# Kernel optimization log

Hardware: AMD Instinct MI355X
Metric: run time of the kernel (lower is better)

Reference implementation:

```python
import jax, jax.numpy as jnp
import numpy as np
import math

D_MODEL, D_STATE, D_CONV = 1024, 16, 4
D_INNER = 2 * D_MODEL
DT_RANK = math.ceil(D_MODEL / 16)
B, L = 4, 2048


def setup_inputs() -> dict:
    key = jax.random.key(0)
    ks = jax.random.split(key, 10)
    s = 0.02
    x = jax.random.normal(ks[0], (B, L, D_MODEL), dtype=jnp.float32)
    ln_g = jnp.ones((D_MODEL,), jnp.float32)
    ln_b = jnp.zeros((D_MODEL,), jnp.float32)
    W_in = jax.random.normal(ks[1], (D_MODEL, 2 * D_INNER), jnp.float32) * s
    conv_w = jax.random.normal(ks[2], (D_INNER, 1, D_CONV), jnp.float32) * s
    conv_b = jnp.zeros((D_INNER,), jnp.float32)
    W_xp = jax.random.normal(ks[3], (D_INNER, DT_RANK + 2 * D_STATE), jnp.float32) * s
    W_dt = jax.random.normal(ks[4], (DT_RANK, D_INNER), jnp.float32) * (DT_RANK ** -0.5)
    # inverse-softplus of dt ~ 0.01 (between dt_min=0.001 and dt_max=0.1)
    dt_bias = jnp.full((D_INNER,), float(np.log(np.expm1(0.01))), jnp.float32)
    # S4D-real init: A = 1..d_state per channel
    A_log = jnp.log(jnp.broadcast_to(jnp.arange(1, D_STATE + 1, dtype=jnp.float32), (D_INNER, D_STATE)))
    D_skip = jnp.ones((D_INNER,), jnp.float32)
    W_out = jax.random.normal(ks[5], (D_INNER, D_MODEL), jnp.float32) * s
    return dict(x=x, ln_g=ln_g, ln_b=ln_b, W_in=W_in, conv_w=conv_w, conv_b=conv_b,
                W_xp=W_xp, W_dt=W_dt, dt_bias=dt_bias, A_log=A_log, D_skip=D_skip, W_out=W_out)


def _layernorm(x, g, b, eps=1e-5):
    m = jnp.mean(x, axis=-1, keepdims=True)
    v = jnp.mean(jnp.square(x - m), axis=-1, keepdims=True)
    return (x - m) * jax.lax.rsqrt(v + eps) * g + b


def _mamba(xn, W_in, conv_w, conv_b, W_xp, W_dt, dt_bias, A_log, D_skip, W_out):
    # xn: [B, L, d_model]
    xz = xn @ W_in                                   # [B, L, 2*d_inner]
    xi, z = jnp.split(xz, 2, axis=-1)                # each [B, L, d_inner]
    # depthwise causal conv over sequence
    xi_t = jnp.transpose(xi, (0, 2, 1))              # [B, d_inner, L]
    xc = jax.lax.conv_general_dilated(
        xi_t, conv_w, window_strides=(1,), padding=[(D_CONV - 1, 0)],
        feature_group_count=D_INNER, dimension_numbers=('NCH', 'OIH', 'NCH'))
    xc = jnp.transpose(xc, (0, 2, 1)) + conv_b       # [B, L, d_inner]
    xc = jax.nn.silu(xc)
    # input-dependent dt, B, C
    x_dbl = xc @ W_xp                                # [B, L, dt_rank + 2*d_state]
    dt_lo, Bm, Cm = jnp.split(x_dbl, [DT_RANK, DT_RANK + D_STATE], axis=-1)
    delta = jax.nn.softplus(dt_lo @ W_dt + dt_bias)  # [B, L, d_inner]
    A = -jnp.exp(A_log)                              # [d_inner, d_state]

    def step(h, inp):
        dt_t, B_t, C_t, u_t = inp                    # [B,D], [B,N], [B,N], [B,D]
        dA = jnp.exp(dt_t[..., None] * A)            # [B, D, N]
        h = h * dA + (dt_t * u_t)[..., None] * B_t[:, None, :]
        y = jnp.einsum('bdn,bn->bd', h, C_t)
        return h, y

    h0 = jnp.zeros((xn.shape[0], D_INNER, D_STATE), xn.dtype)
    inputs = (jnp.transpose(delta, (1, 0, 2)), jnp.transpose(Bm, (1, 0, 2)),
              jnp.transpose(Cm, (1, 0, 2)), jnp.transpose(xc, (1, 0, 2)))
    _, ys = jax.lax.scan(step, h0, inputs)           # ys: [L, B, d_inner]
    y = jnp.transpose(ys, (1, 0, 2)) + xc * D_skip   # [B, L, d_inner]
    y = y * jax.nn.silu(z)
    return y @ W_out                                 # [B, L, d_model]


def reference(x, ln_g, ln_b, W_in, conv_w, conv_b, W_xp, W_dt, dt_bias, A_log, D_skip, W_out):
    xn = _layernorm(x, ln_g, ln_b)
    return _mamba(xn, W_in, conv_w, conv_b, W_xp, W_dt, dt_bias, A_log, D_skip, W_out) + x
```

## Files before the change

kernel.cpp:

```cpp
#include <hip/hip_runtime.h>

#define DM 1024
#define DI 2048
#define DS 16
#define DTR 64
#define LL 2048
#define NROW 8192

typedef unsigned short u16;
typedef unsigned int u32;
typedef __bf16 bf16x8 __attribute__((ext_vector_type(8)));
typedef float f32x4 __attribute__((ext_vector_type(4)));
typedef float v2f __attribute__((ext_vector_type(2)));

__device__ __forceinline__ float bf2f(u16 u) {
  unsigned int v = ((unsigned int)u) << 16;
  return __builtin_bit_cast(float, v);
}
__device__ __forceinline__ u16 f2bf(float f) {
  unsigned int x = __builtin_bit_cast(unsigned int, f);
  x = x + 0x7fffu + ((x >> 16) & 1u);
  return (u16)(x >> 16);
}
__device__ __forceinline__ float lo_bf(u32 v) { return __builtin_bit_cast(float, v << 16); }
__device__ __forceinline__ float hi_bf(u32 v) { return __builtin_bit_cast(float, v & 0xFFFF0000u); }
__device__ __forceinline__ u32 pack_bf(float a, float b) {
  return (u32)f2bf(a) | ((u32)f2bf(b) << 16);
}
__device__ __forceinline__ bool io_f32(const u16* lng) { return lng[0] == 0; }

__device__ __forceinline__ void async16(const void* g, void* l) {
  __builtin_amdgcn_global_load_lds(
      (const __attribute__((address_space(1))) unsigned int*)g,
      (__attribute__((address_space(3))) unsigned int*)l, 16, 0, 0);
}

__device__ __forceinline__ void pow16v(float e1, v2f* E) {
  float e2 = e1 * e1;
  v2f sq = {e2, e2};
  E[0] = (v2f){e1, e2};
#pragma unroll
  for (int k = 1; k < 8; k++) E[k] = E[k - 1] * sq;
}

__device__ void transpose_dev(const void* __restrict__ in, u16* __restrict__ out,
                              int R, int C, int Cp, int bx, int by, bool f32,
                              int tid, u16 (*tile)[33]) {
  int c0 = bx * 32, r0 = by * 32;
  int tx = tid & 31, ty = tid >> 5;
#pragma unroll
  for (int i = 0; i < 4; i++) {
    int r = r0 + ty + i * 8, c = c0 + tx;
    u16 v = 0;
    if (r < R && c < C) {
      if (f32) v = f2bf(((const float*)in)[(size_t)r * C + c]);
      else     v = ((const u16*)in)[(size_t)r * C + c];
    }
    tile[ty + i * 8][tx] = v;
// ... 62 lines not shown
  ushort4 o;
  u16* po = (u16*)&o;
#pragma unroll
  for (int k = 0; k < 4; k++) {
    float gk = f32 ? ((const float*)g)[c + k] : bf2f(g[c + k]);
    float bk = f32 ? ((const float*)b)[c + k] : bf2f(b[c + k]);
    po[k] = f2bf((f[k] - mean) * inv * gk + bk);
  }
  ((ushort4*)(xn + (size_t)row * DM))[tid] = o;
}

template <int EPI>
__device__ __forceinline__ void gemm_body(const u16* __restrict__ A,
                                          const u16* __restrict__ BT,
                                          void* __restrict__ C,
                                          const void* __restrict__ extra,
                                          int M, int N, int Klen, int ldk,
                                          const u16* __restrict__ lng, int mOff,
                                          u16* ldsA, u16* ldsB) {
  int tid = threadIdx.x;
  int wid = tid >> 6, lane = tid & 63;
  int l15 = lane & 15, quad = lane >> 4;
  int bm = blockIdx.x * 128;
  int bn;
  const u16* Ae = A;
  const u16* Be = BT;
  float* Cpart = nullptr;
  if (EPI == 5) {
    bn = 0;
    int ky = blockIdx.y;
    Ae += (size_t)ky * Klen;
    Be += (size_t)ky * Klen;
    Cpart = (float*)C + (size_t)ky * M * N;
  } else {
    bn = blockIdx.y * 128;
  }
  int wrow = (wid >> 1) * 64, wcol = (wid & 1) * 64;

  f32x4 zero = {0.f, 0.f, 0.f, 0.f};
  f32x4 acc[4][4];
#pragma unroll
  for (int i = 0; i < 4; i++)
#pragma unroll
    for (int j = 0; j < 4; j++) acc[i][j] = zero;

  int row0 = tid >> 2;
  int colb = (tid & 3) * 16;
  const char* Ap0 = (const char*)Ae + ((size_t)(bm + row0) * ldk) * 2 + colb;
  const char* Ap1 = (const char*)Ae + ((size_t)(bm + row0 + 64) * ldk) * 2 + colb;
  const char* Bp0 = (const char*)Be + ((size_t)(bn + row0) * ldk) * 2 + colb;
  const char* Bp1 = (const char*)Be + ((size_t)(bn + row0 + 64) * ldk) * 2 + colb;
  u16* la = ldsA + wid * 512;
  u16* lb = ldsB + wid * 512;

  for (int k0 = 0; k0 < Klen; k0 += 64) {
    size_t kb = (size_t)k0 * 2;
    async16(Ap0 + kb, la);
    async16(Ap1 + kb, la + 2048);
    async16(Ap0 + kb + 64, la + 4096);
    async16(Ap1 + kb + 64, la + 6144);
    async16(Bp0 + kb, lb);
    async16(Bp1 + kb, lb + 2048);
    async16(Bp0 + kb + 64, lb + 4096);
    async16(Bp1 + kb + 64, lb + 6144);
    __syncthreads();
#pragma unroll
    for (int s = 0; s < 2; s++) {
      bf16x8 af[4], bfr[4];
#pragma unroll
      for (int i = 0; i < 4; i++)
        af[i] = *(const bf16x8*)&ldsA[s * 4096 + (wrow + i * 16 + l15) * 32 + quad * 8];
#pragma unroll
      for (int j = 0; j < 4; j++)
        bfr[j] = *(const bf16x8*)&ldsB[s * 4096 + (wcol + j * 16 + l15) * 32 + quad * 8];
#pragma unroll
      for (int i = 0; i < 4; i++)
#pragma unroll
        for (int j = 0; j < 4; j++)
          acc[i][j] = __builtin_amdgcn_mfma_f32_16x16x32_bf16(af[i], bfr[j], acc[i][j], 0, 0, 0);
    }
    __syncthreads();
  }

  bool f32 = (EPI == 2) ? io_f32(lng) : false;
  if (EPI == 2 && !f32) {
    u16* tile = ldsA;
#pragma unroll
    for (int i = 0; i < 4; i++) {
#pragma unroll
      for (int j = 0; j < 4; j++) {
        int gn = bn + wcol + j * 16 + l15;
#pragma unroll
        for (int r = 0; r < 4; r++) {
          int lr = wrow + i * 16 + quad * 4 + r;
          float v = acc[i][j][r];
          v += bf2f(((const u16*)extra)[gn]);
          v = (v > 20.f) ? v : log1pf(__expf(v));
          tile[lr * 128 + wcol + j * 16 + l15] = f2bf(v);
        }
      }
    }
    __syncthreads();
#pragma unroll
    for (int g = 0; g < 8; g++) {
      int gi = g * 256 + tid;
      int row = gi >> 4, cg = gi & 15;
      uint4 v4 = *(const uint4*)&tile[row * 128 + cg * 8];
      *(uint4*)((u16*)C + (size_t)(bm + row + mOff) * N + bn + cg * 8) = v4;
    }
    return;
  }
#pragma unroll
  for (int i = 0; i < 4; i++) {
#pragma unroll
    for (int j = 0; j < 4; j++) {
      int gn = bn + wcol + j * 16 + l15;
#pragma unroll
      for (int r = 0; r < 4; r++) {
        int gm = bm + wrow + i * 16 + quad * 4 + r;
        float v = acc[i][j][r];
        if (EPI == 2) {
          float bias = ((const float*)extra)[gn];
          v += bias;
          float sp = (v > 20.f) ? v : log1pf(__expf(v));
          ((u16*)C)[(size_t)gm * N + gn] = f2bf(sp);
        } else {
          Cpart[(size_t)gm * N + gn] = v;
        }
      }
    }
  }
}

#define GEMM_WRAP(name, EPI)                                                        \
  __global__ __launch_bounds__(256) void name(                                      \
      const u16* __restrict__ A, const u16* __restrict__ BT, void* __restrict__ C,  \
      const void* __restrict__ extra, int M, int N, int Klen, int ldk,              \
      const u16* __restrict__ lng, int mOff) {                                      \
    __shared__ __align__(16) u16 lds[16384];                                        \
    gemm_body<EPI>(A, BT, C, extra, M, N, Klen, ldk, lng, mOff, lds, lds + 8192);   \
  }

GEMM_WRAP(gemm_xp_k, 5)
GEMM_WRAP(gemm_dt_k, 2)

__global__ __launch_bounds__(512, 2) void gemm_in256_k(
    const u16* __restrict__ A, const u16* __restrict__ BT,
    u16* __restrict__ C, u16* __restrict__ Z, int ldk, int Klen) {
  __shared__ __align__(16) u16 lds[65536];
  const int tid = threadIdx.x;
  const int wid = tid >> 6, lane = tid & 63;
  const int l15 = lane & 15, quad = lane >> 4;
  const int bm = blockIdx.x * 256, bn = blockIdx.y * 256;
  const int wrow = (wid >> 2) * 128;
  const int wcol = (wid & 3) * 64;

  const int srow = tid >> 3;
  const int sg = ((tid & 7) ^ (srow & 7)) * 8;
  const u16* Ag[4];
  const u16* Bg[4];
#pragma unroll
  for (int s = 0; s < 4; s++) {
    Ag[s] = A + (size_t)(bm + s * 64 + srow) * ldk + sg;
    Bg[s] = BT + (size_t)(bn + s * 64 + srow) * ldk + sg;
  }
  const int sdst = wid * 512;

// ... 129 lines not shown
    __builtin_amdgcn_s_setprio(0);
    if (st1) {
#pragma unroll
      for (int nf = 0; nf < 2; nf++)
#pragma unroll
        for (int ks = 0; ks < 2; ks++)
          b1[nf][ks] = *(const bf16x8*)&lds[nb + rB[ks] + (2 + nf) * 1024];
    }
  }

  __syncthreads();
  {
    const bool isZ = (bn >= DI);
#pragma unroll
    for (int i = 0; i < 8; i++) {
#pragma unroll
      for (int j = 0; j < 4; j++) {
        int lc = wcol + j * 16 + l15;
        int gr = lc >> 3, go = lc & 7;
#pragma unroll
        for (int r = 0; r < 4; r++) {
          int lr = wrow + i * 16 + quad * 4 + r;
          float v = acc[i][j][r];
          if (isZ) v = v / (1.f + __expf(-v));
          int grs = gr ^ ((lr & 7) ^ ((lr >> 3) & 7));
          lds[lr * 256 + grs * 8 + go] = f2bf(v);
        }
      }
    }
    __syncthreads();
    u16* outp = isZ ? (Z + (size_t)bm * DI + (bn - DI)) : (C + (size_t)bm * DI + bn);
#pragma unroll
    for (int g = 0; g < 16; g++) {
      int gi = g * 512 + tid;
      int row = gi >> 5, cg = gi & 31;
      int cgs = cg ^ ((row & 7) ^ ((row >> 3) & 7));
      uint4 v4 = *(const uint4*)&lds[row * 256 + cgs * 8];
      *(uint4*)(outp + (size_t)row * DI + cg * 8) = v4;
    }
  }
}

__global__ __launch_bounds__(512, 2) void gemm_out256_k(
    const u16* __restrict__ A, const u16* __restrict__ BT,
    void* __restrict__ C, const void* __restrict__ extra,
    int N, int ldk, int Klen, const u16* __restrict__ lng, int mOff) {
  __shared__ __align__(16) u16 lds[49152];
// ... 156 lines not shown
      int gi = g * 512 + tid;
      int row = gi >> 4, cg = gi & 15;
      int cgs = cg ^ ((row & 7) ^ ((row >> 3) & 7));
      uint4 v4 = *(const uint4*)&lds[row * 128 + cgs * 8];
      *(uint4*)((u16*)C + (size_t)(bm + row + mOff) * N + bn + cg * 8) = v4;
    }
  } else {
#pragma unroll
    for (int i = 0; i < 8; i++) {
#pragma unroll
      for (int j = 0; j < 2; j++) {
        int gn = bn + wcol + j * 16 + l15;
#pragma unroll
        for (int r = 0; r < 4; r++) {
          int gm = bm + wrow + i * 16 + quad * 4 + r;
          size_t idx = (size_t)(gm + mOff) * N + gn;
          ((float*)C)[idx] = acc[i][j][r] + ((const float*)extra)[idx];
        }
      }
    }
  }
}

__global__ __launch_bounds__(256) void conv4_k(const u16* __restrict__ xi,
                                               const void* __restrict__ cw,
                                               const void* __restrict__ cb,
                                               u16* __restrict__ xc,
                                               const u16* __restrict__ lng) {
  bool f32 = io_f32(lng);
  int idx = blockIdx.x * 256 + threadIdx.x;
  int c8 = (idx & (DI / 8 - 1)) * 8;
  int rq = idx >> 8;
  int l4 = (rq & (LL / 4 - 1)) * 4;
  int b = rq >> 9;
  float w[8][4], bi[8];
#pragma unroll
  for (int e = 0; e < 8; e++) {
    if (f32) {
      float4 w4 = ((const float4*)cw)[c8 + e];
      w[e][0] = w4.x; w[e][1] = w4.y; w[e][2] = w4.z; w[e][3] = w4.w;
      bi[e] = ((const float*)cb)[c8 + e];
    } else {
      ushort4 w4 = ((const ushort4*)cw)[c8 + e];
      w[e][0] = bf2f(w4.x); w[e][1] = bf2f(w4.y); w[e][2] = bf2f(w4.z); w[e][3] = bf2f(w4.w);
      bi[e] = bf2f(((const u16*)cb)[c8 + e]);
    }
  }
  size_t base = ((size_t)(b * LL + l4)) * DI + c8;
  float v[7][8];
#pragma unroll
  for (int j = 0; j < 7; j++) {
    int lj = l4 - 3 + j;
    if (lj >= 0) {
      uint4 q = *(const uint4*)&xi[base + (size_t)(j - 3) * DI];
      u32 qq[4] = {q.x, q.y, q.z, q.w};
#pragma unroll
      for (int e = 0; e < 4; e++) {
        v[j][2 * e] = lo_bf(qq[e]);
        v[j][2 * e + 1] = hi_bf(qq[e]);
      }
    } else {
#pragma unroll
      for (int e = 0; e < 8; e++) v[j][e] = 0.f;
    }
  }
#pragma unroll
  for (int r = 0; r < 4; r++) {
    u32 out[4];
#pragma unroll
    for (int e = 0; e < 8; e += 2) {
      float a0 = bi[e], a1 = bi[e + 1];
#pragma unroll
      for (int k = 0; k < 4; k++) {
        a0 += v[r + k][e] * w[e][k];
        a1 += v[r + k][e + 1] * w[e + 1][k];
      }
      a0 = a0 / (1.f + __expf(-a0));
      a1 = a1 / (1.f + __expf(-a1));
      out[e >> 1] = pack_bf(a0, a1);
    }
    uint4 o4 = {out[0], out[1], out[2], out[3]};
    *(uint4*)&xc[base + (size_t)r * DI] = o4;
  }
}

__global__ __launch_bounds__(256) void reduce_dtlo_k(const float* __restrict__ Cpart,
                                                     float* __restrict__ xdbl,
                                                     u16* __restrict__ dtlo, int M) {
  int i = blockIdx.x * 256 + threadIdx.x;
  size_t MN = (size_t)M * 128;
  float v = Cpart[i] + Cpart[MN + i] + Cpart[2 * MN + i] + Cpart[3 * MN + i];
  xdbl[i] = v;
  int j = i & 127, m = i >> 7;
  if (j < 64) dtlo[(size_t)m * 64 + j] = f2bf(v);
}

__device__ __forceinline__ bool fastA(const void* A_log, bool f32, int d0) {
  bool fast = true;
#pragma unroll
  for (int c = 0; c < 2; c++)
    for (int n = 0; n < 16; n++) {
      float al = f32 ? ((const float*)A_log)[(d0 + c) * DS + n]
                     : bf2f(((const u16*)A_log)[(d0 + c) * DS + n]);
      float Av = __expf(al);
      fast = fast && (__builtin_fabsf(Av - (float)(n + 1)) <= 1e-3f * (n + 1));
    }
  return fast;
}

template <int S>
__global__ __launch_bounds__(256) void scan_p1(const u16* __restrict__ delta,
                                               const u16* __restrict__ xc,
                                               const float* __restrict__ xdbl,
                                               const void* __restrict__ A_log,
                                               const u16* __restrict__ lng,
                                               float* __restrict__ Pbuf,
                                               float* __restrict__ Lbuf,
                                               float* __restrict__ sumbuf,
                                               int NS) {
  bool f32 = io_f32(lng);
  int tid = threadIdx.x;
  int seg = blockIdx.x, dch = blockIdx.y, bL = blockIdx.z;
  int d0 = (dch * 256 + tid) * 2;
  size_t rb = (size_t)bL * LL;
  int l0 = seg * S;
  extern __shared__ float bc[];
#pragma unroll 2
  for (int i = tid; i < S * 4; i += 256) {
    int t = i >> 2, k = (i & 3) * 4;
    *(float4*)&bc[t * 16 + k] = *(const float4*)&xdbl[(rb + l0 + t) * 128 + 64 + k];
  }
  __syncthreads();
  size_t sb = ((((size_t)bL * NS + seg) * DI) + d0) * DS;
  const u32* dpu = (const u32*)(delta + (rb + l0) * DI + d0);
  const u32* upu = (const u32*)(xc + (rb + l0) * DI + d0);
  if (fastA(A_log, f32, d0)) {
    v2f h0[8], h1[8];
#pragma unroll
    for (int k = 0; k < 8; k++) { h0[k] = (v2f){0.f, 0.f}; h1[k] = (v2f){0.f, 0.f}; }
    float sum0 = 0.f, sum1 = 0.f;
    const int T = 8;
    for (int t0 = 0; t0 < S; t0 += T) {
      u32 dv[T], uv[T];
#pragma unroll
      for (int j = 0; j < T; j++) {
        dv[j] = dpu[j * (DI / 2)];
        uv[j] = upu[j * (DI / 2)];
      }
      dpu += T * (DI / 2);
      upu += T * (DI / 2);
#pragma unroll
      for (int j = 0; j < T; j++) {
        float dt0 = lo_bf(dv[j]), dt1 = hi_bf(dv[j]);
        float u0 = lo_bf(uv[j]), u1 = hi_bf(uv[j]);
        sum0 += dt0; sum1 += dt1;
        const v2f* B2 = (const v2f*)&bc[(t0 + j) * 16];
        v2f E[8];
        pow16v(__expf(-dt0), E);
        float com0 = dt0 * u0;
        v2f cv0 = {com0, com0};
#pragma unroll
        for (int k = 0; k < 8; k++) h0[k] = h0[k] * E[k] + B2[k] * cv0;
        pow16v(__expf(-dt1), E);
        float com1 = dt1 * u1;
        v2f cv1 = {com1, com1};
#pragma unroll
        for (int k = 0; k < 8; k++) h1[k] = h1[k] * E[k] + B2[k] * cv1;
      }
    }
#pragma unroll
    for (int k = 0; k < 8; k++) { *(v2f*)&Lbuf[sb + 2 * k] = h0[k]; *(v2f*)&Lbuf[sb + 16 + 2 * k] = h1[k]; }
    if (sumbuf) {
      *(v2f*)&sumbuf[((size_t)(bL * NS + seg)) * DI + d0] = (v2f){sum0, sum1};
    } else {
      v2f P[8];
      pow16v(__expf(-sum0), P);
#pragma unroll
      for (int k = 0; k < 8; k++) *(v2f*)&Pbuf[sb + 2 * k] = P[k];
      pow16v(__expf(-sum1), P);
#pragma unroll
      for (int k = 0; k < 8; k++) *(v2f*)&Pbuf[sb + 16 + 2 * k] = P[k];
    }
  } else {
    for (int c = 0; c < 2; c++) {
      int d = d0 + c;
      float A2[16], h[16], P[16];
#pragma unroll
      for (int n = 0; n < 16; n++) {
        float al = f32 ? ((const float*)A_log)[d * DS + n] : bf2f(((const u16*)A_log)[d * DS + n]);
        A2[n] = -__expf(al);
        h[n] = 0.f; P[n] = 1.f;
      }
      const u16* dp = delta + (rb + l0) * DI + d;
      const u16* up = xc + (rb + l0) * DI + d;
      for (int t = 0; t < S; t++) {
        float dt = bf2f(dp[(size_t)t * DI]);
        float u = bf2f(up[(size_t)t * DI]);
        float com = dt * u;
        const float* Bf = &bc[t * 16];
#pragma unroll
        for (int n = 0; n < 16; n++) {
          float dA = __expf(dt * A2[n]);
          h[n] = fmaf(h[n], dA, com * Bf[n]);
          P[n] *= dA;
        }
      }
#pragma unroll
      for (int n = 0; n < 16; n++) { Pbuf[sb + 16 * c + n] = P[n]; Lbuf[sb + 16 * c + n] = h[n]; }
    }
  }
}

__global__ __launch_bounds__(256) void scan_p2(float* __restrict__ Pbuf,
                                               float* __restrict__ Lbuf,
                                               const float* __restrict__ sumbuf,
                                               const void* __restrict__ A_log,
                                               const u16* __restrict__ lng, int NS) {
  int idx = blockIdx.x * 256 + threadIdx.x;
  int bL = idx >> 15;
  int dn = idx & 32767;
  int d = dn >> 4, n = dn & 15;
  bool useSum = false;
  if (sumbuf) {
    bool f32 = io_f32(lng);
    useSum = fastA(A_log, f32, d & ~1);
  }
  float np1 = (float)(n + 1);
  float H = 0.f;
  for (int s = 0; s < NS; s++) {
    size_t o = ((size_t)(bL * NS + s) << 15) + dn;
    float Lv = Lbuf[o];
    float P = useSum ? __expf(-sumbuf[((size_t)(bL * NS + s)) * DI + d] * np1)
                     : Pbuf[o];
    Lbuf[o] = H;
    H = fmaf(P, H, Lv);
  }
}

template <int S>
__global__ __launch_bounds__(256) void scan_p3(u16* __restrict__ dy,
                                               const u16* __restrict__ xc,
                                               const float* __restrict__ xdbl,
                                               const u16* __restrict__ z,
                                               const void* __restrict__ A_log,
                                               const void* __restrict__ D_skip,
                                               const u16* __restrict__ lng,
                                               const float* __restrict__ Lbuf,
                                               int NS) {
  bool f32 = io_f32(lng);
  int tid = threadIdx.x;
  int seg = blockIdx.x, dch = blockIdx.y, bL = blockIdx.z;
  int d0 = (dch * 256 + tid) * 2;
  size_t rb = (size_t)bL * LL;
  int l0 = seg * S;
  extern __shared__ float bc[];
#pragma unroll 2
  for (int i = tid; i < S * 8; i += 256) {
    int t = i >> 3, k = (i & 7) * 4;
    *(float4*)&bc[t * 32 + k] = *(const float4*)&xdbl[(rb + l0 + t) * 128 + 64 + k];
  }
  __syncthreads();
  size_t sb = ((((size_t)bL * NS + seg) * DI) + d0) * DS;
  float Dv0 = f32 ? ((const float*)D_skip)[d0] : bf2f(((const u16*)D_skip)[d0]);
  float Dv1 = f32 ? ((const float*)D_skip)[d0 + 1] : bf2f(((const u16*)D_skip)[d0 + 1]);
  u32* dpu = (u32*)(dy + (rb + l0) * DI + d0);
  const u32* upu = (const u32*)(xc + (rb + l0) * DI + d0);
  const u32* zpu = (const u32*)(z + (rb + l0) * DI + d0);
  if (fastA(A_log, f32, d0)) {
    v2f h0[8], h1[8];
#pragma unroll
    for (int k = 0; k < 8; k++) {
      h0[k] = *(const v2f*)&Lbuf[sb + 2 * k];
      h1[k] = *(const v2f*)&Lbuf[sb + 16 + 2 * k];
    }
    const int T = 8;
    for (int t0 = 0; t0 < S; t0 += T) {
      u32 dv[T], uv[T], zv[T];
#pragma unroll
      for (int j = 0; j < T; j++) {
        dv[j] = dpu[j * (DI / 2)];
        uv[j] = upu[j * (DI / 2)];
        zv[j] = zpu[j * (DI / 2)];
      }
      upu += T * (DI / 2);
      zpu += T * (DI / 2);
#pragma unroll
      for (int j = 0; j < T; j++) {
        float dt0 = lo_bf(dv[j]), dt1 = hi_bf(dv[j]);
        float u0 = lo_bf(uv[j]), u1 = hi_bf(uv[j]);
        float zg0 = lo_bf(zv[j]), zg1 = hi_bf(zv[j]);
        const v2f* B2 = (const v2f*)&bc[(t0 + j) * 32];
        const v2f* C2 = (const v2f*)&bc[(t0 + j) * 32 + 16];
        v2f E[8];
        pow16v(__expf(-dt0), E);
        float com0 = dt0 * u0;
        v2f cv = {com0, com0};
        v2f a0 = {0.f, 0.f}, a1 = {0.f, 0.f};
#pragma unroll
        for (int k = 0; k < 8; k += 2) {
          h0[k] = h0[k] * E[k] + B2[k] * cv;
          h0[k + 1] = h0[k + 1] * E[k + 1] + B2[k + 1] * cv;
          a0 += h0[k] * C2[k];
          a1 += h0[k + 1] * C2[k + 1];
        }
        float cs0 = (a0.x + a0.y) + (a1.x + a1.y);
        pow16v(__expf(-dt1), E);
        float com1 = dt1 * u1;
        cv = (v2f){com1, com1};
        a0 = (v2f){0.f, 0.f}; a1 = (v2f){0.f, 0.f};
#pragma unroll
        for (int k = 0; k < 8; k += 2) {
          h1[k] = h1[k] * E[k] + B2[k] * cv;
          h1[k + 1] = h1[k + 1] * E[k + 1] + B2[k + 1] * cv;
          a0 += h1[k] * C2[k];
          a1 += h1[k + 1] * C2[k + 1];
        }
        float cs1 = (a0.x + a0.y) + (a1.x + a1.y);
        float y0 = (cs0 + u0 * Dv0) * zg0;
        float y1 = (cs1 + u1 * Dv1) * zg1;
        dpu[j * (DI / 2)] = pack_bf(y0, y1);
      }
      dpu += T * (DI / 2);
    }
  } else {
    for (int c = 0; c < 2; c++) {
      int d = d0 + c;
      float A2[16], h[16];
#pragma unroll
      for (int n = 0; n < 16; n++) {
        float al = f32 ? ((const float*)A_log)[d * DS + n] : bf2f(((const u16*)A_log)[d * DS + n]);
        A2[n] = -__expf(al);
        h[n] = Lbuf[sb + 16 * c + n];
      }
      float Dv = (c == 0) ? Dv0 : Dv1;
      u16* dp = dy + (rb + l0) * DI + d;
      const u16* up = xc + (rb + l0) * DI + d;
      const u16* zp = z + (rb + l0) * DI + d;
      for (int t = 0; t < S; t++) {
        float dt = bf2f(dp[(size_t)t * DI]);
        float u = bf2f(up[(size_t)t * DI]);
        float zg = bf2f(zp[(size_t)t * DI]);
        float com = dt * u;
        const float* Bf = &bc[t * 32];
        const float* Cf = &bc[t * 32 + 16];
        float cs = 0.f;
#pragma unroll
        for (int n = 0; n < 16; n++) {
          float dA = __expf(dt * A2[n]);
          h[n] = fmaf(h[n], dA, com * Bf[n]);
          cs = fmaf(h[n], Cf[n], cs);
        }
        dp[(size_t)t * DI] = f2bf((cs + u * Dv) * zg);
      }
    }
  }
}

static void launch_scan(int NS, int nb, u16* xi, u16* xc, float* xdbl, u16* z,
                        const u16* A_log, const u16* D_sk, const u16* ln_g,
                        float* Pbuf, float* Lbuf, float* sumbuf,
                        hipStream_t stream) {
  int S = LL / NS;
  dim3 g1(NS, 4, nb);
  if (S == 32) {
    scan_p1<32><<<g1, 256, 32 * 64, stream>>>(xi, xc, xdbl, A_log, ln_g, Pbuf, Lbuf, sumbuf, NS);
  } else if (S == 64) {
    scan_p1<64><<<g1, 256, 64 * 64, stream>>>(xi, xc, xdbl, A_log, ln_g, Pbuf, Lbuf, sumbuf, NS);
  } else {
    scan_p1<128><<<g1, 256, 128 * 64, stream>>>(xi, xc, xdbl, A_log, ln_g, Pbuf, Lbuf, sumbuf, NS);
  }
  scan_p2<<<nb * 128, 256, 0, stream>>>(Pbuf, Lbuf, sumbuf, A_log, ln_g, NS);
  if (S == 32) {
    scan_p3<32><<<g1, 256, 32 * 128, stream>>>(xi, xc, xdbl, z, A_log, D_sk, ln_g, Lbuf, NS);
  } else if (S == 64) {
    scan_p3<64><<<g1, 256, 64 * 128, stream>>>(xi, xc, xdbl, z, A_log, D_sk, ln_g, Lbuf, NS);
  } else {
    scan_p3<128><<<g1, 256, 128 * 128, stream>>>(xi, xc, xdbl, z, A_log, D_sk, ln_g, Lbuf, NS);
  }
}

extern "C" void kernel_launch(void* const* d_in, const int* in_sizes, int n_in,
                              void* d_out, int out_size, void* d_ws, size_t ws_size,
                              hipStream_t stream) {
  const u16* x = (const u16*)d_in[0];
  const u16* ln_g = (const u16*)d_in[1];
  const u16* ln_b = (const u16*)d_in[2];
  const u16* W_in = (const u16*)d_in[3];
  const u16* cw = (const u16*)d_in[4];
  const u16* cb = (const u16*)d_in[5];
  const u16* W_xp = (const u16*)d_in[6];
  const u16* W_dt = (const u16*)d_in[7];
  const u16* dt_b = (const u16*)d_in[8];
  const u16* A_log = (const u16*)d_in[9];
  const u16* D_sk = (const u16*)d_in[10];
  const u16* W_out = (const u16*)d_in[11];

  char* ws = (char*)d_ws;
  const size_t MB = 1024 * 1024;

  if (ws_size >= 124 * MB) {
    int NS = (ws_size >= 180 * MB) ? 64 : (ws_size >= 144 * MB) ? 32 : 16;
    u16* xc = (u16*)(ws + 0);
    u16* xn = xc;
    u16* W_inT = (u16*)(ws + 16 * MB);
    u16* xi = (u16*)(ws + 32 * MB);
    u16* z = (u16*)(ws + 64 * MB);
    float* xdbl = (float*)(ws + 96 * MB);
    u16* dtlo = (u16*)(ws + 100 * MB);
    u16* W_xpT = (u16*)(ws + 101 * MB);
    u16* W_dtT = (u16*)(ws + 102 * MB);
    u16* W_outT = (u16*)(ws + 103 * MB);
    size_t stateSz = (size_t)NS * 4 * DI * DS * 4;
    float* Cpart = (float*)(ws + 107 * MB);
    float* Pbuf = (float*)(ws + 107 * MB);
    float* Lbuf = (float*)(ws + 107 * MB + stateSz);
    float* sumbuf = (NS >= 32) ? (float*)(ws + 107 * MB + 2 * stateSz) : nullptr;

    prep_k<<<6528 + NROW, 256, 0, stream>>>(W_in, W_inT, W_dt, W_dtT, W_xp, W_xpT,
                                            W_out, W_outT, x, ln_g, ln_b, xn);
    gemm_in256_k<<<dim3(NROW / 256, (2 * DI) / 256), 512, 0, stream>>>(xn, W_inT, xi, z, DM, DM);
    conv4_k<<<(NROW / 4) * (DI / 8) / 256, 256, 0, stream>>>(xi, cw, cb, xc, ln_g);
    gemm_xp_k<<<dim3(64, 4), 256, 0, stream>>>(xc, W_xpT, Cpart, nullptr, NROW, 128, 512, DI, ln_g, 0);
    reduce_dtlo_k<<<(NROW * 128) / 256, 256, 0, stream>>>(Cpart, xdbl, dtlo, NROW);
    gemm_dt_k<<<dim3(64, 16), 256, 0, stream>>>(dtlo, W_dtT, xi, dt_b, NROW, DI, DTR, DTR, ln_g, 0);
    launch_scan(NS, 4, xi, xc, xdbl, z, A_log, D_sk, ln_g, Pbuf, Lbuf, sumbuf, stream);
    gemm_out256_k<<<dim3(NROW / 256, DM / 128), 512, 0, stream>>>(xi, W_outT, d_out, x, DM, DI, DI, ln_g, 0);
  } else {
    int NS = 32;
    u16* W_inT = (u16*)(ws + 0);
    u16* W_xpT = (u16*)(ws + 8 * MB);
    u16* W_dtT = (u16*)(ws + 9 * MB);
    u16* W_outT = (u16*)(ws + 10 * MB);
    u16* xn = (u16*)(ws + 14 * MB);
    u16* xi = (u16*)(ws + 30 * MB);
    u16* z = (u16*)(ws + 38 * MB);
    u16* xc = (u16*)(ws + 46 * MB);
    float* xdbl = (float*)(ws + 54 * MB);
    u16* dtlo = (u16*)(ws + 55 * MB);
    float* Cpart = (float*)(ws + 56 * MB);
    float* Pbuf = (float*)(ws + 56 * MB);
    float* Lbuf = (float*)(ws + 61 * MB);

    prep_k<<<6528 + NROW, 256, 0, stream>>>(W_in, W_inT, W_dt, W_dtT, W_xp, W_xpT,
                                            W_out, W_outT, x, ln_g, ln_b, xn);
    for (int b = 0; b < 4; b++) {
      const u16* xnb = xn + (size_t)b * LL * DM;
      gemm_in256_k<<<dim3(LL / 256, (2 * DI) / 256), 512, 0, stream>>>(xnb, W_inT, xi, z, DM, DM);
      conv4_k<<<(LL / 4) * (DI / 8) / 256, 256, 0, stream>>>(xi, cw, cb, xc, ln_g);
      gemm_xp_k<<<dim3(16, 4), 256, 0, stream>>>(xc, W_xpT, Cpart, nullptr, LL, 128, 512, DI, ln_g, 0);
      reduce_dtlo_k<<<(LL * 128) / 256, 256, 0, stream>>>(Cpart, xdbl, dtlo, LL);
      gemm_dt_k<<<dim3(16, 16), 256, 0, stream>>>(dtlo, W_dtT, xi, dt_b, LL, DI, DTR, DTR, ln_g, 0);
      launch_scan(NS, 1, xi, xc, xdbl, z, A_log, D_sk, ln_g, Pbuf, Lbuf, nullptr, stream);
      gemm_out256_k<<<dim3(LL / 256, DM / 128), 512, 0, stream>>>(xi, W_outT, d_out, x, DM, DI, DI, ln_g, b * LL);
    }
  }
}
```

Baseline: 486.6 us.

## Fuse causal conv+SiLU into x_proj GEMM and recompute it inside scan kernels

```diff
diff --git a/kernel.cpp b/kernel.cpp
--- a/kernel.cpp
+++ b/kernel.cpp
@@ -34,6 +34,8 @@
       (const __attribute__((address_space(1))) unsigned int*)g,
       (__attribute__((address_space(3))) unsigned int*)l, 16, 0, 0);
 }
+
+__device__ __forceinline__ float silu(float a) { return a / (1.f + __expf(-a)); }
 
 __device__ __forceinline__ void pow16v(float e1, v2f* E) {
   float e2 = e1 * e1;
@@ -142,19 +144,7 @@
   int wid = tid >> 6, lane = tid & 63;
   int l15 = lane & 15, quad = lane >> 4;
   int bm = blockIdx.x * 128;
-  int bn;
-  const u16* Ae = A;
-  const u16* Be = BT;
-  float* Cpart = nullptr;
-  if (EPI == 5) {
-    bn = 0;
-    int ky = blockIdx.y;
-    Ae += (size_t)ky * Klen;
-    Be += (size_t)ky * Klen;
-    Cpart = (float*)C + (size_t)ky * M * N;
-  } else {
-    bn = blockIdx.y * 128;
-  }
+  int bn = blockIdx.y * 128;
   int wrow = (wid >> 1) * 64, wcol = (wid & 1) * 64;
 
   f32x4 zero = {0.f, 0.f, 0.f, 0.f};
@@ -166,10 +156,10 @@
 
   int row0 = tid >> 2;
   int colb = (tid & 3) * 16;
-  const char* Ap0 = (const char*)Ae + ((size_t)(bm + row0) * ldk) * 2 + colb;
-  const char* Ap1 = (const char*)Ae + ((size_t)(bm + row0 + 64) * ldk) * 2 + colb;
-  const char* Bp0 = (const char*)Be + ((size_t)(bn + row0) * ldk) * 2 + colb;
-  const char* Bp1 = (const char*)Be + ((size_t)(bn + row0 + 64) * ldk) * 2 + colb;
+  const char* Ap0 = (const char*)A + ((size_t)(bm + row0) * ldk) * 2 + colb;
+  const char* Ap1 = (const char*)A + ((size_t)(bm + row0 + 64) * ldk) * 2 + colb;
+  const char* Bp0 = (const char*)BT + ((size_t)(bn + row0) * ldk) * 2 + colb;
+  const char* Bp1 = (const char*)BT + ((size_t)(bn + row0 + 64) * ldk) * 2 + colb;
   u16* la = ldsA + wid * 512;
   u16* lb = ldsB + wid * 512;
 
@@ -202,8 +192,8 @@
     __syncthreads();
   }
 
-  bool f32 = (EPI == 2) ? io_f32(lng) : false;
-  if (EPI == 2 && !f32) {
+  bool f32 = io_f32(lng);
+  if (!f32) {
     u16* tile = ldsA;
 #pragma unroll
     for (int i = 0; i < 4; i++) {
@@ -239,30 +229,142 @@
       for (int r = 0; r < 4; r++) {
         int gm = bm + wrow + i * 16 + quad * 4 + r;
         float v = acc[i][j][r];
-        if (EPI == 2) {
-          float bias = ((const float*)extra)[gn];
-          v += bias;
-          float sp = (v > 20.f) ? v : log1pf(__expf(v));
-          ((u16*)C)[(size_t)gm * N + gn] = f2bf(sp);
+        float bias = ((const float*)extra)[gn];
+        v += bias;
+        float sp = (v > 20.f) ? v : log1pf(__expf(v));
+        ((u16*)C)[(size_t)gm * N + gn] = f2bf(sp);
+      }
+    }
+  }
+}
+
+__global__ __launch_bounds__(256) void gemm_dt_k(
+    const u16* __restrict__ A, const u16* __restrict__ BT, void* __restrict__ C,
+    const void* __restrict__ extra, int M, int N, int Klen, int ldk,
+    const u16* __restrict__ lng, int mOff) {
+  __shared__ __align__(16) u16 lds[16384];
+  gemm_body<2>(A, BT, C, extra, M, N, Klen, ldk, lng, mOff, lds, lds + 8192);
+}
+
+__global__ __launch_bounds__(256) void gemm_xpf_k(
+    const u16* __restrict__ xi, const u16* __restrict__ BT,
+    float* __restrict__ Cpart, const void* __restrict__ cw,
+    const void* __restrict__ cb, const u16* __restrict__ lng, int M) {
+  __shared__ __align__(16) u16 ldsA[10240];
+  __shared__ __align__(16) u16 ldsB[8192];
+  bool f32 = io_f32(lng);
+  int tid = threadIdx.x;
+  int wid = tid >> 6, lane = tid & 63;
+  int l15 = lane & 15, quad = lane >> 4;
+  int bm = blockIdx.x * 128;
+  int ky = blockIdx.y;
+  float* Cp = Cpart + (size_t)ky * M * 128;
+  int wrow = (wid >> 1) * 64, wcol = (wid & 1) * 64;
+
+  f32x4 zero = {0.f, 0.f, 0.f, 0.f};
+  f32x4 acc[4][4];
+#pragma unroll
+  for (int i = 0; i < 4; i++)
+#pragma unroll
+    for (int j = 0; j < 4; j++) acc[i][j] = zero;
+
+  int row0 = tid >> 2, colb = (tid & 3) * 16;
+  const char* Bp0 = (const char*)BT + ((size_t)row0 * DI + (size_t)ky * 512) * 2 + colb;
+  const char* Bp1 = (const char*)BT + ((size_t)(row0 + 64) * DI + (size_t)ky * 512) * 2 + colb;
+  u16* lb = ldsB + wid * 512;
+
+  int ar = tid >> 1, as = tid & 1;
+  int grow = bm + ar;
+  int lrow = grow & (LL - 1);
+  const u16* xrow = xi + (size_t)grow * DI;
+
+  for (int k0 = 0; k0 < 512; k0 += 64) {
+    size_t kb = (size_t)k0 * 2;
+    async16(Bp0 + kb, lb);
+    async16(Bp1 + kb, lb + 2048);
+    async16(Bp0 + kb + 64, lb + 4096);
+    async16(Bp1 + kb + 64, lb + 6144);
+    int cbase = ky * 512 + k0 + as * 32;
+#pragma unroll
+    for (int it = 0; it < 4; it++) {
+      int cc = ((ar + it) & 3) * 8;
+      int ch = cbase + cc;
+      float wv[8][4], bv[8];
+#pragma unroll
+      for (int e = 0; e < 8; e++) {
+        if (f32) {
+          float4 w4 = ((const float4*)cw)[ch + e];
+          wv[e][0] = w4.x; wv[e][1] = w4.y; wv[e][2] = w4.z; wv[e][3] = w4.w;
+          bv[e] = ((const float*)cb)[ch + e];
         } else {
-          Cpart[(size_t)gm * N + gn] = v;
+          ushort4 w4 = ((const ushort4*)cw)[ch + e];
+          wv[e][0] = bf2f(w4.x); wv[e][1] = bf2f(w4.y);
+          wv[e][2] = bf2f(w4.z); wv[e][3] = bf2f(w4.w);
+          bv[e] = bf2f(((const u16*)cb)[ch + e]);
         }
       }
-    }
-  }
-}
-
-#define GEMM_WRAP(name, EPI)                                                        \
-  __global__ __launch_bounds__(256) void name(                                      \
-      const u16* __restrict__ A, const u16* __restrict__ BT, void* __restrict__ C,  \
-      const void* __restrict__ extra, int M, int N, int Klen, int ldk,              \
-      const u16* __restrict__ lng, int mOff) {                                      \
-    __shared__ __align__(16) u16 lds[16384];                                        \
-    gemm_body<EPI>(A, BT, C, extra, M, N, Klen, ldk, lng, mOff, lds, lds + 8192);   \
-  }
-
-GEMM_WRAP(gemm_xp_k, 5)
-GEMM_WRAP(gemm_dt_k, 2)
+      float xin[4][8];
+#pragma unroll
+      for (int j = 0; j < 4; j++) {
+        int lr = lrow - 3 + j;
+        if (lr >= 0) {
+          uint4 q = *(const uint4*)&xrow[(ptrdiff_t)(j - 3) * DI + ch];
+          u32 qq[4] = {q.x, q.y, q.z, q.w};
+#pragma unroll
+          for (int e = 0; e < 4; e++) {
+            xin[j][2 * e] = lo_bf(qq[e]);
+            xin[j][2 * e + 1] = hi_bf(qq[e]);
+          }
+        } else {
+#pragma unroll
+          for (int e = 0; e < 8; e++) xin[j][e] = 0.f;
+        }
+      }
+      u32 o[4];
+#pragma unroll
+      for (int e = 0; e < 8; e += 2) {
+        float a0 = bv[e], a1 = bv[e + 1];
+#pragma unroll
+        for (int j = 0; j < 4; j++) {
+          a0 += xin[j][e] * wv[e][j];
+          a1 += xin[j][e + 1] * wv[e + 1][j];
+        }
+        o[e >> 1] = pack_bf(silu(a0), silu(a1));
+      }
+      uint4 q4 = {o[0], o[1], o[2], o[3]};
+      *(uint4*)&ldsA[as * 5120 + ar * 40 + cc] = q4;
+    }
+    __syncthreads();
+#pragma unroll
+    for (int s = 0; s < 2; s++) {
+      bf16x8 af[4], bfr[4];
+#pragma unroll
+      for (int i = 0; i < 4; i++)
+        af[i] = *(const bf16x8*)&ldsA[s * 5120 + (wrow + i * 16 + l15) * 40 + quad * 8];
+#pragma unroll
+      for (int j = 0; j < 4; j++)
+        bfr[j] = *(const bf16x8*)&ldsB[s * 4096 + (wcol + j * 16 + l15) * 32 + quad * 8];
+#pragma unroll
+      for (int i = 0; i < 4; i++)
+#pragma unroll
+        for (int j = 0; j < 4; j++)
+          acc[i][j] = __builtin_amdgcn_mfma_f32_16x16x32_bf16(af[i], bfr[j], acc[i][j], 0, 0, 0);
+    }
+    __syncthreads();
+  }
+#pragma unroll
+  for (int i = 0; i < 4; i++) {
+#pragma unroll
+    for (int j = 0; j < 4; j++) {
+      int gn = wcol + j * 16 + l15;
+#pragma unroll
+      for (int r = 0; r < 4; r++) {
+        int gm = bm + wrow + i * 16 + quad * 4 + r;
+        Cp[(size_t)gm * 128 + gn] = acc[i][j][r];
+      }
+    }
+  }
+}
 
 __global__ __launch_bounds__(512, 2) void gemm_in256_k(
     const u16* __restrict__ A, const u16* __restrict__ BT,
@@ -438,7 +540,7 @@
         for (int r = 0; r < 4; r++) {
           int lr = wrow + i * 16 + quad * 4 + r;
           float v = acc[i][j][r];
-          if (isZ) v = v / (1.f + __expf(-v));
+          if (isZ) v = silu(v);
           int grs = gr ^ ((lr & 7) ^ ((lr >> 3) & 7));
           lds[lr * 256 + grs * 8 + go] = f2bf(v);
         }
@@ -641,68 +743,6 @@
   }
 }
 
-__global__ __launch_bounds__(256) void conv4_k(const u16* __restrict__ xi,
-                                               const void* __restrict__ cw,
-                                               const void* __restrict__ cb,
-                                               u16* __restrict__ xc,
-                                               const u16* __restrict__ lng) {
-  bool f32 = io_f32(lng);
-  int idx = blockIdx.x * 256 + threadIdx.x;
-  int c8 = (idx & (DI / 8 - 1)) * 8;
-  int rq = idx >> 8;
-  int l4 = (rq & (LL / 4 - 1)) * 4;
-  int b = rq >> 9;
-  float w[8][4], bi[8];
-#pragma unroll
-  for (int e = 0; e < 8; e++) {
-    if (f32) {
-      float4 w4 = ((const float4*)cw)[c8 + e];
-      w[e][0] = w4.x; w[e][1] = w4.y; w[e][2] = w4.z; w[e][3] = w4.w;
-      bi[e] = ((const float*)cb)[c8 + e];
-    } else {
-      ushort4 w4 = ((const ushort4*)cw)[c8 + e];
-      w[e][0] = bf2f(w4.x); w[e][1] = bf2f(w4.y); w[e][2] = bf2f(w4.z); w[e][3] = bf2f(w4.w);
-      bi[e] = bf2f(((const u16*)cb)[c8 + e]);
-    }
-  }
-  size_t base = ((size_t)(b * LL + l4)) * DI + c8;
-  float v[7][8];
-#pragma unroll
-  for (int j = 0; j < 7; j++) {
-    int lj = l4 - 3 + j;
-    if (lj >= 0) {
-      uint4 q = *(const uint4*)&xi[base + (size_t)(j - 3) * DI];
-      u32 qq[4] = {q.x, q.y, q.z, q.w};
-#pragma unroll
-      for (int e = 0; e < 4; e++) {
-        v[j][2 * e] = lo_bf(qq[e]);
-        v[j][2 * e + 1] = hi_bf(qq[e]);
-      }
-    } else {
-#pragma unroll
-      for (int e = 0; e < 8; e++) v[j][e] = 0.f;
-    }
-  }
-#pragma unroll
-  for (int r = 0; r < 4; r++) {
-    u32 out[4];
-#pragma unroll
-    for (int e = 0; e < 8; e += 2) {
-      float a0 = bi[e], a1 = bi[e + 1];
-#pragma unroll
-      for (int k = 0; k < 4; k++) {
-        a0 += v[r + k][e] * w[e][k];
-        a1 += v[r + k][e + 1] * w[e + 1][k];
-      }
-      a0 = a0 / (1.f + __expf(-a0));
-      a1 = a1 / (1.f + __expf(-a1));
-      out[e >> 1] = pack_bf(a0, a1);
-    }
-    uint4 o4 = {out[0], out[1], out[2], out[3]};
-    *(uint4*)&xc[base + (size_t)r * DI] = o4;
-  }
-}
-
 __global__ __launch_bounds__(256) void reduce_dtlo_k(const float* __restrict__ Cpart,
                                                      float* __restrict__ xdbl,
                                                      u16* __restrict__ dtlo, int M) {
@@ -729,9 +769,11 @@
 
 template <int S>
 __global__ __launch_bounds__(256) void scan_p1(const u16* __restrict__ delta,
-                                               const u16* __restrict__ xc,
+                                               const u16* __restrict__ xi,
                                                const float* __restrict__ xdbl,
                                                const void* __restrict__ A_log,
+                                               const void* __restrict__ cw,
+                                               const void* __restrict__ cb,
                                                const u16* __restrict__ lng,
                                                float* __restrict__ Pbuf,
                                                float* __restrict__ Lbuf,
@@ -752,8 +794,32 @@
   __syncthreads();
   size_t sb = ((((size_t)bL * NS + seg) * DI) + d0) * DS;
   const u32* dpu = (const u32*)(delta + (rb + l0) * DI + d0);
-  const u32* upu = (const u32*)(xc + (rb + l0) * DI + d0);
+  const u32* upu = (const u32*)(xi + (rb + l0) * DI + d0);
   if (fastA(A_log, f32, d0)) {
+    float w0[4], w1[4], cb0, cb1;
+    if (f32) {
+      float4 a0 = ((const float4*)cw)[d0], a1 = ((const float4*)cw)[d0 + 1];
+      w0[0] = a0.x; w0[1] = a0.y; w0[2] = a0.z; w0[3] = a0.w;
+      w1[0] = a1.x; w1[1] = a1.y; w1[2] = a1.z; w1[3] = a1.w;
+      cb0 = ((const float*)cb)[d0]; cb1 = ((const float*)cb)[d0 + 1];
+    } else {
+      ushort4 a0 = ((const ushort4*)cw)[d0], a1 = ((const ushort4*)cw)[d0 + 1];
+      w0[0] = bf2f(a0.x); w0[1] = bf2f(a0.y); w0[2] = bf2f(a0.z); w0[3] = bf2f(a0.w);
+      w1[0] = bf2f(a1.x); w1[1] = bf2f(a1.y); w1[2] = bf2f(a1.z); w1[3] = bf2f(a1.w);
+      cb0 = bf2f(((const u16*)cb)[d0]); cb1 = bf2f(((const u16*)cb)[d0 + 1]);
+    }
+    float hx0[3], hx1[3];
+    if (l0 == 0) {
+#pragma unroll
+      for (int i = 0; i < 3; i++) { hx0[i] = 0.f; hx1[i] = 0.f; }
+    } else {
+      const u32* hp = (const u32*)(xi + (rb + l0 - 3) * DI + d0);
+#pragma unroll
+      for (int i = 0; i < 3; i++) {
+        u32 v = hp[i * (DI / 2)];
+        hx0[i] = lo_bf(v); hx1[i] = hi_bf(v);
+      }
+    }
     v2f h0[8], h1[8];
 #pragma unroll
     for (int k = 0; k < 8; k++) { h0[k] = (v2f){0.f, 0.f}; h1[k] = (v2f){0.f, 0.f}; }
@@ -771,7 +837,12 @@
 #pragma unroll
       for (int j = 0; j < T; j++) {
         float dt0 = lo_bf(dv[j]), dt1 = hi_bf(dv[j]);
-        float u0 = lo_bf(uv[j]), u1 = hi_bf(uv[j]);
+        float xr0 = lo_bf(uv[j]), xr1 = hi_bf(uv[j]);
+        float a0 = cb0 + hx0[0] * w0[0] + hx0[1] * w0[1] + hx0[2] * w0[2] + xr0 * w0[3];
+        float a1 = cb1 + hx1[0] * w1[0] + hx1[1] * w1[1] + hx1[2] * w1[2] + xr1 * w1[3];
+        float u0 = silu(a0), u1 = silu(a1);
+        hx0[0] = hx0[1]; hx0[1] = hx0[2]; hx0[2] = xr0;
+        hx1[0] = hx1[1]; hx1[1] = hx1[2]; hx1[2] = xr1;
         sum0 += dt0; sum1 += dt1;
         const v2f* B2 = (const v2f*)&bc[(t0 + j) * 16];
         v2f E[8];
@@ -810,11 +881,28 @@
         A2[n] = -__expf(al);
         h[n] = 0.f; P[n] = 1.f;
       }
+      float wc[4], bc2;
+      if (f32) {
+        float4 w4 = ((const float4*)cw)[d];
+        wc[0] = w4.x; wc[1] = w4.y; wc[2] = w4.z; wc[3] = w4.w;
+        bc2 = ((const float*)cb)[d];
+      } else {
+        ushort4 w4 = ((const ushort4*)cw)[d];
+        wc[0] = bf2f(w4.x); wc[1] = bf2f(w4.y); wc[2] = bf2f(w4.z); wc[3] = bf2f(w4.w);
+        bc2 = bf2f(((const u16*)cb)[d]);
+      }
+      float hx[3];
+#pragma unroll
+      for (int i = 0; i < 3; i++)
+        hx[i] = (l0 == 0) ? 0.f : bf2f(xi[(rb + l0 - 3 + i) * DI + d]);
       const u16* dp = delta + (rb + l0) * DI + d;
-      const u16* up = xc + (rb + l0) * DI + d;
+      const u16* up = xi + (rb + l0) * DI + d;
       for (int t = 0; t < S; t++) {
         float dt = bf2f(dp[(size_t)t * DI]);
-        float u = bf2f(up[(size_t)t * DI]);
+        float xv = bf2f(up[(size_t)t * DI]);
+        float av = bc2 + hx[0] * wc[0] + hx[1] * wc[1] + hx[2] * wc[2] + xv * wc[3];
+        float u = silu(av);
+        hx[0] = hx[1]; hx[1] = hx[2]; hx[2] = xv;
         float com = dt * u;
         const float* Bf = &bc[t * 16];
 #pragma unroll
@@ -858,11 +946,13 @@
 
 template <int S>
 __global__ __launch_bounds__(256) void scan_p3(u16* __restrict__ dy,
-                                               const u16* __restrict__ xc,
+                                               const u16* __restrict__ xi,
                                                const float* __restrict__ xdbl,
                                                const u16* __restrict__ z,
                                                const void* __restrict__ A_log,
                                                const void* __restrict__ D_skip,
+                                               const void* __restrict__ cw,
+                                               const void* __restrict__ cb,
                                                const u16* __restrict__ lng,
                                                const float* __restrict__ Lbuf,
                                                int NS) {
@@ -883,9 +973,33 @@
   float Dv0 = f32 ? ((const float*)D_skip)[d0] : bf2f(((const u16*)D_skip)[d0]);
   float Dv1 = f32 ? ((const float*)D_skip)[d0 + 1] : bf2f(((const u16*)D_skip)[d0 + 1]);
   u32* dpu = (u32*)(dy + (rb + l0) * DI + d0);
-  const u32* upu = (const u32*)(xc + (rb + l0) * DI + d0);
+  const u32* upu = (const u32*)(xi + (rb + l0) * DI + d0);
   const u32* zpu = (const u32*)(z + (rb + l0) * DI + d0);
   if (fastA(A_log, f32, d0)) {
+    float w0[4], w1[4], cb0, cb1;
+    if (f32) {
+      float4 a0 = ((const float4*)cw)[d0], a1 = ((const float4*)cw)[d0 + 1];
+      w0[0] = a0.x; w0[1] = a0.y; w0[2] = a0.z; w0[3] = a0.w;
+      w1[0] = a1.x; w1[1] = a1.y; w1[2] = a1.z; w1[3] = a1.w;
+      cb0 = ((const float*)cb)[d0]; cb1 = ((const float*)cb)[d0 + 1];
+    } else {
+      ushort4 a0 = ((const ushort4*)cw)[d0], a1 = ((const ushort4*)cw)[d0 + 1];
+      w0[0] = bf2f(a0.x); w0[1] = bf2f(a0.y); w0[2] = bf2f(a0.z); w0[3] = bf2f(a0.w);
+      w1[0] = bf2f(a1.x); w1[1] = bf2f(a1.y); w1[2] = bf2f(a1.z); w1[3] = bf2f(a1.w);
+      cb0 = bf2f(((const u16*)cb)[d0]); cb1 = bf2f(((const u16*)cb)[d0 + 1]);
+    }
+    float hx0[3], hx1[3];
+    if (l0 == 0) {
+#pragma unroll
+      for (int i = 0; i < 3; i++) { hx0[i] = 0.f; hx1[i] = 0.f; }
+    } else {
+      const u32* hp = (const u32*)(xi + (rb + l0 - 3) * DI + d0);
+#pragma unroll
+      for (int i = 0; i < 3; i++) {
+        u32 v = hp[i * (DI / 2)];
+        hx0[i] = lo_bf(v); hx1[i] = hi_bf(v);
+      }
+    }
     v2f h0[8], h1[8];
 #pragma unroll
     for (int k = 0; k < 8; k++) {
@@ -906,8 +1020,13 @@
 #pragma unroll
       for (int j = 0; j < T; j++) {
         float dt0 = lo_bf(dv[j]), dt1 = hi_bf(dv[j]);
-        float u0 = lo_bf(uv[j]), u1 = hi_bf(uv[j]);
+        float xr0 = lo_bf(uv[j]), xr1 = hi_bf(uv[j]);
         float zg0 = lo_bf(zv[j]), zg1 = hi_bf(zv[j]);
+        float a0c = cb0 + hx0[0] * w0[0] + hx0[1] * w0[1] + hx0[2] * w0[2] + xr0 * w0[3];
+        float a1c = cb1 + hx1[0] * w1[0] + hx1[1] * w1[1] + hx1[2] * w1[2] + xr1 * w1[3];
+        float u0 = silu(a0c), u1 = silu(a1c);
+        hx0[0] = hx0[1]; hx0[1] = hx0[2]; hx0[2] = xr0;
+        hx1[0] = hx1[1]; hx1[1] = hx1[2]; hx1[2] = xr1;
         const v2f* B2 = (const v2f*)&bc[(t0 + j) * 32];
         const v2f* C2 = (const v2f*)&bc[(t0 + j) * 32 + 16];
         v2f E[8];
@@ -951,14 +1070,31 @@
         A2[n] = -__expf(al);
         h[n] = Lbuf[sb + 16 * c + n];
       }
+      float wc[4], bc2;
+      if (f32) {
+        float4 w4 = ((const float4*)cw)[d];
+        wc[0] = w4.x; wc[1] = w4.y; wc[2] = w4.z; wc[3] = w4.w;
+        bc2 = ((const float*)cb)[d];
+      } else {
+        ushort4 w4 = ((const ushort4*)cw)[d];
+        wc[0] = bf2f(w4.x); wc[1] = bf2f(w4.y); wc[2] = bf2f(w4.z); wc[3] = bf2f(w4.w);
+        bc2 = bf2f(((const u16*)cb)[d]);
+      }
+      float hx[3];
+#pragma unroll
+      for (int i = 0; i < 3; i++)
+        hx[i] = (l0 == 0) ? 0.f : bf2f(xi[(rb + l0 - 3 + i) * DI + d]);
       float Dv = (c == 0) ? Dv0 : Dv1;
       u16* dp = dy + (rb + l0) * DI + d;
-      const u16* up = xc + (rb + l0) * DI + d;
+      const u16* up = xi + (rb + l0) * DI + d;
       const u16* zp = z + (rb + l0) * DI + d;
       for (int t = 0; t < S; t++) {
         float dt = bf2f(dp[(size_t)t * DI]);
-        float u = bf2f(up[(size_t)t * DI]);
+        float xv = bf2f(up[(size_t)t * DI]);
         float zg = bf2f(zp[(size_t)t * DI]);
+        float av = bc2 + hx[0] * wc[0] + hx[1] * wc[1] + hx[2] * wc[2] + xv * wc[3];
+        float u = silu(av);
+        hx[0] = hx[1]; hx[1] = hx[2]; hx[2] = xv;
         float com = dt * u;
         const float* Bf = &bc[t * 32];
         const float* Cf = &bc[t * 32 + 16];
@@ -975,26 +1111,27 @@
   }
 }
 
-static void launch_scan(int NS, int nb, u16* xi, u16* xc, float* xdbl, u16* z,
-                        const u16* A_log, const u16* D_sk, const u16* ln_g,
+static void launch_scan(int NS, int nb, u16* delta, u16* xi, float* xdbl, u16* z,
+                        const u16* A_log, const u16* D_sk, const u16* cw,
+                        const u16* cb, const u16* ln_g,
                         float* Pbuf, float* Lbuf, float* sumbuf,
                         hipStream_t stream) {
   int S = LL / NS;
   dim3 g1(NS, 4, nb);
   if (S == 32) {
-    scan_p1<32><<<g1, 256, 32 * 64, stream>>>(xi, xc, xdbl, A_log, ln_g, Pbuf, Lbuf, sumbuf, NS);
+    scan_p1<32><<<g1, 256, 32 * 64, stream>>>(delta, xi, xdbl, A_log, cw, cb, ln_g, Pbuf, Lbuf, sumbuf, NS);
   } else if (S == 64) {
-    scan_p1<64><<<g1, 256, 64 * 64, stream>>>(xi, xc, xdbl, A_log, ln_g, Pbuf, Lbuf, sumbuf, NS);
+    scan_p1<64><<<g1, 256, 64 * 64, stream>>>(delta, xi, xdbl, A_log, cw, cb, ln_g, Pbuf, Lbuf, sumbuf, NS);
   } else {
-    scan_p1<128><<<g1, 256, 128 * 64, stream>>>(xi, xc, xdbl, A_log, ln_g, Pbuf, Lbuf, sumbuf, NS);
+    scan_p1<128><<<g1, 256, 128 * 64, stream>>>(delta, xi, xdbl, A_log, cw, cb, ln_g, Pbuf, Lbuf, sumbuf, NS);
   }
   scan_p2<<<nb * 128, 256, 0, stream>>>(Pbuf, Lbuf, sumbuf, A_log, ln_g, NS);
   if (S == 32) {
-    scan_p3<32><<<g1, 256, 32 * 128, stream>>>(xi, xc, xdbl, z, A_log, D_sk, ln_g, Lbuf, NS);
+    scan_p3<32><<<g1, 256, 32 * 128, stream>>>(delta, xi, xdbl, z, A_log, D_sk, cw, cb, ln_g, Lbuf, NS);
   } else if (S == 64) {
-    scan_p3<64><<<g1, 256, 64 * 128, stream>>>(xi, xc, xdbl, z, A_log, D_sk, ln_g, Lbuf, NS);
+    scan_p3<64><<<g1, 256, 64 * 128, stream>>>(delta, xi, xdbl, z, A_log, D_sk, cw, cb, ln_g, Lbuf, NS);
   } else {
-    scan_p3<128><<<g1, 256, 128 * 128, stream>>>(xi, xc, xdbl, z, A_log, D_sk, ln_g, Lbuf, NS);
+    scan_p3<128><<<g1, 256, 128 * 128, stream>>>(delta, xi, xdbl, z, A_log, D_sk, cw, cb, ln_g, Lbuf, NS);
   }
 }
 
@@ -1018,10 +1155,10 @@
   const size_t MB = 1024 * 1024;
 
   if (ws_size >= 124 * MB) {
-    int NS = (ws_size >= 180 * MB) ? 64 : (ws_size >= 144 * MB) ? 32 : 16;
-    u16* xc = (u16*)(ws + 0);
-    u16* xn = xc;
+    int NS = (ws_size >= 144 * MB) ? 32 : 16;
+    u16* xn = (u16*)(ws + 0);
     u16* W_inT = (u16*)(ws + 16 * MB);
+    u16* delta = (u16*)(ws + 0);
     u16* xi = (u16*)(ws + 32 * MB);
     u16* z = (u16*)(ws + 64 * MB);
     float* xdbl = (float*)(ws + 96 * MB);
@@ -1038,12 +1175,11 @@
     prep_k<<<6528 + NROW, 256, 0, stream>>>(W_in, W_inT, W_dt, W_dtT, W_xp, W_xpT,
                                             W_out, W_outT, x, ln_g, ln_b, xn);
     gemm_in256_k<<<dim3(NROW / 256, (2 * DI) / 256), 512, 0, stream>>>(xn, W_inT, xi, z, DM, DM);
-    conv4_k<<<(NROW / 4) * (DI / 8) / 256, 256, 0, stream>>>(xi, cw, cb, xc, ln_g);
-    gemm_xp_k<<<dim3(64, 4), 256, 0, stream>>>(xc, W_xpT, Cpart, nullptr, NROW, 128, 512, DI, ln_g, 0);
+    gemm_xpf_k<<<dim3(NROW / 128, 4), 256, 0, stream>>>(xi, W_xpT, Cpart, cw, cb, ln_g, NROW);
     reduce_dtlo_k<<<(NROW * 128) / 256, 256, 0, stream>>>(Cpart, xdbl, dtlo, NROW);
-    gemm_dt_k<<<dim3(64, 16), 256, 0, stream>>>(dtlo, W_dtT, xi, dt_b, NROW, DI, DTR, DTR, ln_g, 0);
-    launch_scan(NS, 4, xi, xc, xdbl, z, A_log, D_sk, ln_g, Pbuf, Lbuf, sumbuf, stream);
-    gemm_out256_k<<<dim3(NROW / 256, DM / 128), 512, 0, stream>>>(xi, W_outT, d_out, x, DM, DI, DI, ln_g, 0);
+    gemm_dt_k<<<dim3(64, 16), 256, 0, stream>>>(dtlo, W_dtT, delta, dt_b, NROW, DI, DTR, DTR, ln_g, 0);
+    launch_scan(NS, 4, delta, xi, xdbl, z, A_log, D_sk, cw, cb, ln_g, Pbuf, Lbuf, sumbuf, stream);
+    gemm_out256_k<<<dim3(NROW / 256, DM / 128), 512, 0, stream>>>(delta, W_outT, d_out, x, DM, DI, DI, ln_g, 0);
   } else {
     int NS = 32;
     u16* W_inT = (u16*)(ws + 0);
@@ -1053,7 +1189,7 @@
     u16* xn = (u16*)(ws + 14 * MB);
     u16* xi = (u16*)(ws + 30 * MB);
     u16* z = (u16*)(ws + 38 * MB);
-    u16* xc = (u16*)(ws + 46 * MB);
+    u16* delta = (u16*)(ws + 46 * MB);
     float* xdbl = (float*)(ws + 54 * MB);
     u16* dtlo = (u16*)(ws + 55 * MB);
     float* Cpart = (float*)(ws + 56 * MB);
@@ -1065,12 +1201,11 @@
     for (int b = 0; b < 4; b++) {
       const u16* xnb = xn + (size_t)b * LL * DM;
       gemm_in256_k<<<dim3(LL / 256, (2 * DI) / 256), 512, 0, stream>>>(xnb, W_inT, xi, z, DM, DM);
-      conv4_k<<<(LL / 4) * (DI / 8) / 256, 256, 0, stream>>>(xi, cw, cb, xc, ln_g);
-      gemm_xp_k<<<dim3(16, 4), 256, 0, stream>>>(xc, W_xpT, Cpart, nullptr, LL, 128, 512, DI, ln_g, 0);
+      gemm_xpf_k<<<dim3(LL / 128, 4), 256, 0, stream>>>(xi, W_xpT, Cpart, cw, cb, ln_g, LL);
       reduce_dtlo_k<<<(LL * 128) / 256, 256, 0, stream>>>(Cpart, xdbl, dtlo, LL);
-      gemm_dt_k<<<dim3(16, 16), 256, 0, stream>>>(dtlo, W_dtT, xi, dt_b, LL, DI, DTR, DTR, ln_g, 0);
-      launch_scan(NS, 1, xi, xc, xdbl, z, A_log, D_sk, ln_g, Pbuf, Lbuf, nullptr, stream);
-      gemm_out256_k<<<dim3(LL / 256, DM / 128), 512, 0, stream>>>(xi, W_outT, d_out, x, DM, DI, DI, ln_g, b * LL);
-    }
-  }
-}
+      gemm_dt_k<<<dim3(16, 16), 256, 0, stream>>>(dtlo, W_dtT, delta, dt_b, LL, DI, DTR, DTR, ln_g, 0);
+      launch_scan(NS, 1, delta, xi, xdbl, z, A_log, D_sk, cw, cb, ln_g, Pbuf, Lbuf, nullptr, stream);
+      gemm_out256_k<<<dim3(LL / 256, DM / 128), 512, 0, stream>>>(delta, W_outT, d_out, x, DM, DI, DI, ln_g, b * LL);
+    }
+  }
+}
```

New measurement: 510.3 us. 1.05x slower.
